# Optimization experiments

Measured on AMD Instinct MI355X. Metric: run time of the kernel, lower is better.

Reference implementation:

```python
import jax, jax.numpy as jnp
import numpy as np

B, S, VD, MD = 32, 2048, 512, 512
AD = max(VD, MD)


def setup_inputs() -> dict:
    key = jax.random.key(0)
    k1, k2, k3, k4, k5, k6 = jax.random.split(key, 6)
    query = jax.random.normal(k1, (B, VD), dtype=jnp.float32)
    keys = jax.random.normal(k2, (B, S, MD), dtype=jnp.float32)
    mask = jax.random.randint(k3, (B, S), 0, 2).astype(jnp.bool_)
    # torch Linear weight layout: [out, in]
    W1 = jax.random.normal(k4, (AD, VD), dtype=jnp.float32) * (1.0 / np.sqrt(VD))
    W2 = jax.random.normal(k5, (AD, MD), dtype=jnp.float32) * (1.0 / np.sqrt(MD))
    v = jax.random.normal(k6, (AD,), dtype=jnp.float32) * (1.0 / np.sqrt(AD))
    return {"query": query, "keys": keys, "mask": mask, "W1": W1, "W2": W2, "v": v}


def reference(query, keys, mask, W1, W2, v):
    # w1_query: [B, 1, AD]; w2_keys: [B, S, AD]
    w1_query = jnp.einsum('bd,ad->ba', query, W1)[:, None, :]
    w2_keys = jnp.einsum('bsd,ad->bsa', keys, W2)
    combined = jnp.tanh(w1_query + w2_keys)            # [B, S, AD]
    scores = jnp.einsum('bsa,a->bs', combined, v)      # [B, S]
    scores = jnp.where(mask, scores, -jnp.inf)
    attn_weights = jax.nn.softmax(scores, axis=-1)
    return attn_weights
```

## Files before the change

### kernel.cpp

```cpp
#include <hip/hip_runtime.h>
#include <math.h>

#define BB 32
#define SS 2048
#define DD 512
#define AD 512

#define BM 128
#define BN 128
#define BK 64

typedef __bf16 bf16;
typedef __attribute__((ext_vector_type(8))) __bf16 bf16x8;
typedef __attribute__((ext_vector_type(4))) __bf16 bf16x4;
typedef __attribute__((ext_vector_type(4))) float floatx4;

__device__ inline void async16(const void* g, void* l) {
    __builtin_amdgcn_global_load_lds(
        (const __attribute__((address_space(1))) unsigned int*)g,
        (__attribute__((address_space(3))) unsigned int*)l, 16, 0, 0);
}

__global__ void mask_probe_kernel(const unsigned char* __restrict__ m8,
                                  int* __restrict__ flag) {
    int t = threadIdx.x + blockIdx.x * 256;
    int any = 0;
    for (int i = t; i < BB * SS; i += gridDim.x * 256) {
        if ((i & 3) && m8[i]) any = 1;
    }
    if (__any(any)) {
        if ((threadIdx.x & 63) == 0) atomicOr(flag, 1);
    }
}

__global__ void convert_kernel(const float* __restrict__ src,
                               bf16* __restrict__ dst, int n8) {
    int i = threadIdx.x + blockIdx.x * 256;
    if (i >= n8) return;
    const float4* s4 = (const float4*)src + (size_t)i * 2;
    float4 x = s4[0], y = s4[1];
    bf16x8 o;
    o[0] = (bf16)x.x; o[1] = (bf16)x.y; o[2] = (bf16)x.z; o[3] = (bf16)x.w;
    o[4] = (bf16)y.x; o[5] = (bf16)y.y; o[6] = (bf16)y.z; o[7] = (bf16)y.w;
    *(bf16x8*)(dst + (size_t)i * 8) = o;
}

__global__ void w1q_kernel(const float* __restrict__ query,
                           const float* __restrict__ W1,
                           float* __restrict__ w1q) {
    int b = blockIdx.y;
    int a = blockIdx.x * 4 + (threadIdx.x >> 6);
    int lane = threadIdx.x & 63;
    const float4* q4 = (const float4*)(query + (size_t)b * DD) + lane * 2;
    const float4* w4 = (const float4*)(W1 + (size_t)a * DD) + lane * 2;
    float4 qa = q4[0], qb = q4[1];
    float4 wa = w4[0], wb = w4[1];
    float acc = qa.x * wa.x + qa.y * wa.y + qa.z * wa.z + qa.w * wa.w
              + qb.x * wb.x + qb.y * wb.y + qb.z * wb.z + qb.w * wb.w;
#pragma unroll
    for (int off = 32; off > 0; off >>= 1) acc += __shfl_down(acc, off);
    if (lane == 0) w1q[(size_t)b * AD + a] = acc;
}

__global__ __launch_bounds__(256, 4)
void gemm_scores_mfma(const bf16* __restrict__ keysb,
                      const bf16* __restrict__ W2b,
                      const float* __restrict__ w1q,
                      const float* __restrict__ v,
                      float* __restrict__ partial, int tiles_y) {
    __shared__ bf16 a_lds[BM * BK];
    __shared__ bf16 b_lds[BN * BK];
    __shared__ float s_red[BM];

    const int t    = threadIdx.x;
    const int lane = t & 63;
    const int w    = t >> 6;
    const int ml   = lane & 15;
    const int kg   = lane >> 4;
    const int b    = blockIdx.z;
    const int s0   = blockIdx.x * BM;
    const int a0   = blockIdx.y * BN;
    const int m_off = (w & 1) * 64;
    const int n_off = (w >> 1) * 64;

    const bf16* Ablk = keysb + ((size_t)b * SS + s0) * DD;
    const bf16* Bblk = W2b + (size_t)a0 * DD;

    if (t < BM) s_red[t] = 0.f;

    floatx4 acc[4][4];
#pragma unroll
    for (int mi = 0; mi < 4; ++mi)
#pragma unroll
        for (int ni = 0; ni < 4; ++ni)
            acc[mi][ni] = (floatx4)(0.f);

    const int rr = lane >> 3;
    const int cc = lane & 7;

    for (int chunk = 0; chunk < DD / BK; ++chunk) {
        const int d0 = chunk * BK;
#pragma unroll
        for (int i = 0; i < 4; ++i) {
            int r  = w * 32 + i * 8 + rr;
            int cs = cc ^ (r & 7);
            const bf16* ga = Ablk + (size_t)r * DD + d0 + cs * 8;
            const bf16* gb = Bblk + (size_t)r * DD + d0 + cs * 8;
            async16(ga, &a_lds[(w * 32 + i * 8) * BK]);
            async16(gb, &b_lds[(w * 32 + i * 8) * BK]);
        }
        __syncthreads();

#pragma unroll
        for (int ks = 0; ks < 2; ++ks) {
            bf16x8 af[4], bfr[4];
#pragma unroll
            for (int mi = 0; mi < 4; ++mi) {
                int R = m_off + mi * 16 + ml;
                int c = (ks * 4 + kg) ^ (R & 7);
                af[mi] = *(const bf16x8*)&a_lds[R * BK + c * 8];
            }
#pragma unroll
            for (int ni = 0; ni < 4; ++ni) {
                int R = n_off + ni * 16 + ml;
                int c = (ks * 4 + kg) ^ (R & 7);
                bfr[ni] = *(const bf16x8*)&b_lds[R * BK + c * 8];
            }
#pragma unroll
            for (int mi = 0; mi < 4; ++mi)
#pragma unroll
                for (int ni = 0; ni < 4; ++ni)
                    acc[mi][ni] = __builtin_amdgcn_mfma_f32_16x16x32_bf16(
                        af[mi], bfr[ni], acc[mi][ni], 0, 0, 0);
        }
        __syncthreads();
    }

    float w1qa[4], va[4];
#pragma unroll
    for (int ni = 0; ni < 4; ++ni) {
        int a = a0 + n_off + ni * 16 + ml;
        w1qa[ni] = w1q[(size_t)b * AD + a];
        va[ni]   = v[a];
    }
#pragma unroll
    for (int mi = 0; mi < 4; ++mi) {
#pragma unroll
        for (int reg = 0; reg < 4; ++reg) {
            float p = 0.f;
#pragma unroll
            for (int ni = 0; ni < 4; ++ni) {
                float x = acc[mi][ni][reg] + w1qa[ni];
                float th = 1.f - 2.f / (1.f + __expf(2.f * x));
                p = fmaf(th, va[ni], p);
            }
            p += __shfl_xor(p, 1);
            p += __shfl_xor(p, 2);
            p += __shfl_xor(p, 4);
            p += __shfl_xor(p, 8);
            if (ml == 0)
                atomicAdd(&s_red[m_off + mi * 16 + kg * 4 + reg], p);
        }
    }
    __syncthreads();
    if (t < BM)
        partial[(((size_t)b * SS) + s0 + t) * (size_t)tiles_y + blockIdx.y] = s_red[t];
}

#define FBK 32
#define FLDK (FBK + 8)
__global__ __launch_bounds__(256, 2)
void gemm_scores_fallback(const float* __restrict__ keys,
                          const float* __restrict__ W2,
                          const float* __restrict__ w1q,
                          const float* __restrict__ v,
                          float* __restrict__ partial) {
    __shared__ bf16 a_lds[BM][FLDK];
    __shared__ bf16 b_lds[BN][FLDK];
    __shared__ float s_red[BM];

    const int t    = threadIdx.x;
    const int lane = t & 63;
    const int w    = t >> 6;
    const int ml   = lane & 15;
    const int kg   = lane >> 4;
    const int b    = blockIdx.z;
    const int s0   = blockIdx.x * BM;
    const int a0   = blockIdx.y * BN;
    const int m_off = (w & 1) * 64;
    const int n_off = (w >> 1) * 64;

    const float* Ablk = keys + ((size_t)b * SS + s0) * DD;
    const float* Bblk = W2 + (size_t)a0 * DD;

    if (t < BM) s_red[t] = 0.f;

    floatx4 acc[4][4];
#pragma unroll
    for (int mi = 0; mi < 4; ++mi)
#pragma unroll
        for (int ni = 0; ni < 4; ++ni)
            acc[mi][ni] = (floatx4)(0.f);

    float4 ga[4], gb[4];
#pragma unroll
    for (int i = 0; i < 4; ++i) {
        int idx = t + 256 * i;
        int r = idx >> 3, c = idx & 7;
        ga[i] = *(const float4*)(Ablk + (size_t)r * DD + c * 4);
        gb[i] = *(const float4*)(Bblk + (size_t)r * DD + c * 4);
    }

    for (int chunk = 0; chunk < DD / FBK; ++chunk) {
        __syncthreads();
#pragma unroll
        for (int i = 0; i < 4; ++i) {
            int idx = t + 256 * i;
            int r = idx >> 3, c = idx & 7;
            bf16x4 pa, pb;
            pa[0] = (bf16)ga[i].x; pa[1] = (bf16)ga[i].y;
            pa[2] = (bf16)ga[i].z; pa[3] = (bf16)ga[i].w;
            pb[0] = (bf16)gb[i].x; pb[1] = (bf16)gb[i].y;
            pb[2] = (bf16)gb[i].z; pb[3] = (bf16)gb[i].w;
            *(bf16x4*)&a_lds[r][c * 4] = pa;
            *(bf16x4*)&b_lds[r][c * 4] = pb;
        }
        __syncthreads();
        if (chunk < DD / FBK - 1) {
            int d0 = (chunk + 1) * FBK;
#pragma unroll
            for (int i = 0; i < 4; ++i) {
                int idx = t + 256 * i;
                int r = idx >> 3, c = idx & 7;
                ga[i] = *(const float4*)(Ablk + (size_t)r * DD + d0 + c * 4);
                gb[i] = *(const float4*)(Bblk + (size_t)r * DD + d0 + c * 4);
            }
        }
        bf16x8 af[4], bfr[4];
#pragma unroll
        for (int mi = 0; mi < 4; ++mi)
            af[mi] = *(const bf16x8*)&a_lds[m_off + mi * 16 + ml][kg * 8];
#pragma unroll
        for (int ni = 0; ni < 4; ++ni)
            bfr[ni] = *(const bf16x8*)&b_lds[n_off + ni * 16 + ml][kg * 8];
#pragma unroll
        for (int mi = 0; mi < 4; ++mi)
#pragma unroll
            for (int ni = 0; ni < 4; ++ni)
                acc[mi][ni] = __builtin_amdgcn_mfma_f32_16x16x32_bf16(
                    af[mi], bfr[ni], acc[mi][ni], 0, 0, 0);
    }

    float w1qa[4], va[4];
#pragma unroll
    for (int ni = 0; ni < 4; ++ni) {
        int a = a0 + n_off + ni * 16 + ml;
        w1qa[ni] = w1q[(size_t)b * AD + a];
        va[ni]   = v[a];
    }
#pragma unroll
    for (int mi = 0; mi < 4; ++mi) {
#pragma unroll
        for (int reg = 0; reg < 4; ++reg) {
            float p = 0.f;
#pragma unroll
            for (int ni = 0; ni < 4; ++ni) {
                float x = acc[mi][ni][reg] + w1qa[ni];
                float th = 1.f - 2.f / (1.f + __expf(2.f * x));
                p = fmaf(th, va[ni], p);
            }
            p += __shfl_xor(p, 1);
            p += __shfl_xor(p, 2);
            p += __shfl_xor(p, 4);
            p += __shfl_xor(p, 8);
            if (ml == 0)
                atomicAdd(&s_red[m_off + mi * 16 + kg * 4 + reg], p);
        }
    }
    __syncthreads();
    if (t < BM)
        partial[(((size_t)b * SS) + s0 + t) * 4 + blockIdx.y] = s_red[t];
}

__global__ void softmax_kernel(const float* __restrict__ partial,
                               const int* __restrict__ mask_i32,
                               const unsigned char* __restrict__ mask_u8,
                               const int* __restrict__ flag,
                               float* __restrict__ out) {
    const int b = blockIdx.x;
    const int t = threadIdx.x;
    __shared__ float rmax[4], rsum[4];
    const int wid = t >> 6, lane = t & 63;

    float sv[8]; int mv[8];
    const int bytes = (*flag != 0);
#pragma unroll
    for (int k = 0; k < 8; ++k) {
        int i = t + 256 * k;
        float4 p4 = *(const float4*)(partial + ((size_t)b * SS + i) * 4);
        sv[k] = (p4.x + p4.y) + (p4.z + p4.w);
        mv[k] = bytes ? (int)mask_u8[(size_t)b * SS + i]
                      : mask_i32[(size_t)b * SS + i];
    }

    float mx = -INFINITY;
#pragma unroll
    for (int k = 0; k < 8; ++k) mx = fmaxf(mx, mv[k] ? sv[k] : -INFINITY);
#pragma unroll
    for (int off = 32; off > 0; off >>= 1) mx = fmaxf(mx, __shfl_xor(mx, off));
    if (lane == 0) rmax[wid] = mx;
    __syncthreads();
    mx = fmaxf(fmaxf(rmax[0], rmax[1]), fmaxf(rmax[2], rmax[3]));

    float ev[8]; float sum = 0.f;
#pragma unroll
    for (int k = 0; k < 8; ++k) {
        ev[k] = mv[k] ? __expf(sv[k] - mx) : 0.f;
        sum += ev[k];
    }
#pragma unroll
    for (int off = 32; off > 0; off >>= 1) sum += __shfl_xor(sum, off);
    if (lane == 0) rsum[wid] = sum;
    __syncthreads();
    sum = (rsum[0] + rsum[1]) + (rsum[2] + rsum[3]);
    float inv = 1.f / sum;
#pragma unroll
    for (int k = 0; k < 8; ++k)
        out[(size_t)b * SS + t + 256 * k] = ev[k] * inv;
}

extern "C" void kernel_launch(void* const* d_in, const int* in_sizes, int n_in,
                              void* d_out, int out_size, void* d_ws, size_t ws_size,
                              hipStream_t stream) {
    const float* query = (const float*)d_in[0];
    const float* keys  = (const float*)d_in[1];
    const void*  mask  = d_in[2];
    const float* W1    = (const float*)d_in[3];
    const float* W2    = (const float*)d_in[4];
    const float* v     = (const float*)d_in[5];
    float* out = (float*)d_out;

    char* wsb = (char*)d_ws;
    int*   flag    = (int*)wsb;
    float* w1q     = (float*)(wsb + 256);
    float* partial = (float*)(wsb + 256 + 65536);
    bf16*  keysb   = (bf16*)(wsb + 256 + 65536 + 1048576);
    bf16*  W2b     = (bf16*)(wsb + 256 + 65536 + 1048576 + (size_t)BB * SS * DD * 2);
    size_t need = 256 + 65536 + 1048576 + (size_t)BB * SS * DD * 2 + (size_t)AD * DD * 2;

    hipMemsetAsync(flag, 0, 4, stream);
    mask_probe_kernel<<<64, 256, 0, stream>>>((const unsigned char*)mask, flag);
    w1q_kernel<<<dim3(AD / 4, BB), 256, 0, stream>>>(query, W1, w1q);

    if (ws_size >= need) {
        int nk8 = BB * SS * DD / 8;
        int nw8 = AD * DD / 8;
        convert_kernel<<<(nk8 + 255) / 256, 256, 0, stream>>>(keys, keysb, nk8);
        convert_kernel<<<(nw8 + 255) / 256, 256, 0, stream>>>(W2, W2b, nw8);
        gemm_scores_mfma<<<dim3(SS / BM, AD / BN, BB), 256, 0, stream>>>(
            keysb, W2b, w1q, v, partial, AD / BN);
    } else {
        gemm_scores_fallback<<<dim3(SS / BM, AD / BN, BB), 256, 0, stream>>>(
            keys, W2, w1q, v, partial);
    }
    softmax_kernel<<<BB, 256, 0, stream>>>(partial, (const int*)mask,
                                           (const unsigned char*)mask, flag, out);
}
```

Baseline: 266.9 us.

## Double-buffer LDS tiles in MFMA GEMM and reorder grid for A-tile reuse

The MFMA scores GEMM now uses two LDS buffers with a K-chunk of 32, issuing async global-to-LDS loads for the next chunk while computing on the current one. This replaces the previous load-sync-compute pattern, which exposed memory latency on every chunk. The grid is also reordered so that the four AD tiles sharing one keys tile are launched next to each other, which should improve L2 reuse of keys. The costs are more chunk iterations, each with its own barrier, and a hardcoded tiles_y of 4. The loop still has a single barrier per chunk, so it relies on the async LDS writes for chunk c+1 having completed when that barrier is reached.

```diff
diff --git a/kernel.cpp b/kernel.cpp
--- a/kernel.cpp
+++ b/kernel.cpp
@@ -8,7 +8,7 @@
 
 #define BM 128
 #define BN 128
-#define BK 64
+#define BK 32
 
 typedef __bf16 bf16;
 typedef __attribute__((ext_vector_type(8))) __bf16 bf16x8;
@@ -67,9 +67,9 @@
                       const bf16* __restrict__ W2b,
                       const float* __restrict__ w1q,
                       const float* __restrict__ v,
-                      float* __restrict__ partial, int tiles_y) {
-    __shared__ bf16 a_lds[BM * BK];
-    __shared__ bf16 b_lds[BN * BK];
+                      float* __restrict__ partial) {
+    __shared__ bf16 a_lds[2][BM * BK];
+    __shared__ bf16 b_lds[2][BN * BK];
     __shared__ float s_red[BM];
 
     const int t    = threadIdx.x;
@@ -78,8 +78,8 @@
     const int ml   = lane & 15;
     const int kg   = lane >> 4;
     const int b    = blockIdx.z;
-    const int s0   = blockIdx.x * BM;
-    const int a0   = blockIdx.y * BN;
+    const int a0   = blockIdx.x * BN;
+    const int s0   = blockIdx.y * BM;
     const int m_off = (w & 1) * 64;
     const int n_off = (w >> 1) * 64;
 
@@ -95,44 +95,51 @@
         for (int ni = 0; ni < 4; ++ni)
             acc[mi][ni] = (floatx4)(0.f);
 
-    const int rr = lane >> 3;
-    const int cc = lane & 7;
-
-    for (int chunk = 0; chunk < DD / BK; ++chunk) {
-        const int d0 = chunk * BK;
-#pragma unroll
-        for (int i = 0; i < 4; ++i) {
-            int r  = w * 32 + i * 8 + rr;
-            int cs = cc ^ (r & 7);
-            const bf16* ga = Ablk + (size_t)r * DD + d0 + cs * 8;
-            const bf16* gb = Bblk + (size_t)r * DD + d0 + cs * 8;
-            async16(ga, &a_lds[(w * 32 + i * 8) * BK]);
-            async16(gb, &b_lds[(w * 32 + i * 8) * BK]);
-        }
-        __syncthreads();
-
-#pragma unroll
-        for (int ks = 0; ks < 2; ++ks) {
-            bf16x8 af[4], bfr[4];
-#pragma unroll
-            for (int mi = 0; mi < 4; ++mi) {
-                int R = m_off + mi * 16 + ml;
-                int c = (ks * 4 + kg) ^ (R & 7);
-                af[mi] = *(const bf16x8*)&a_lds[R * BK + c * 8];
+    const int NCHUNK = DD / BK;
+
+#pragma unroll
+    for (int i = 0; i < 2; ++i) {
+        int lin = w * 128 + i * 64 + lane;
+        int r = lin >> 2, cc = lin & 3, cs = cc ^ (r & 3);
+        async16(Ablk + (size_t)r * DD + cs * 8, &a_lds[0][(w * 128 + i * 64) * 8]);
+        async16(Bblk + (size_t)r * DD + cs * 8, &b_lds[0][(w * 128 + i * 64) * 8]);
+    }
+    __syncthreads();
+
+    for (int c = 0; c < NCHUNK; ++c) {
+        const int cur = c & 1;
+        if (c + 1 < NCHUNK) {
+            const int d0 = (c + 1) * BK;
+            const int nxt = (c + 1) & 1;
+#pragma unroll
+            for (int i = 0; i < 2; ++i) {
+                int lin = w * 128 + i * 64 + lane;
+                int r = lin >> 2, cc = lin & 3, cs = cc ^ (r & 3);
+                async16(Ablk + (size_t)r * DD + d0 + cs * 8,
+                        &a_lds[nxt][(w * 128 + i * 64) * 8]);
+                async16(Bblk + (size_t)r * DD + d0 + cs * 8,
+                        &b_lds[nxt][(w * 128 + i * 64) * 8]);
             }
-#pragma unroll
-            for (int ni = 0; ni < 4; ++ni) {
-                int R = n_off + ni * 16 + ml;
-                int c = (ks * 4 + kg) ^ (R & 7);
-                bfr[ni] = *(const bf16x8*)&b_lds[R * BK + c * 8];
-            }
-#pragma unroll
-            for (int mi = 0; mi < 4; ++mi)
-#pragma unroll
-                for (int ni = 0; ni < 4; ++ni)
-                    acc[mi][ni] = __builtin_amdgcn_mfma_f32_16x16x32_bf16(
-                        af[mi], bfr[ni], acc[mi][ni], 0, 0, 0);
-        }
+        }
+
+        bf16x8 af[4], bfr[4];
+#pragma unroll
+        for (int mi = 0; mi < 4; ++mi) {
+            int R = m_off + mi * 16 + ml;
+            af[mi] = *(const bf16x8*)&a_lds[cur][R * BK + (kg ^ (R & 3)) * 8];
+        }
+#pragma unroll
+        for (int ni = 0; ni < 4; ++ni) {
+            int R = n_off + ni * 16 + ml;
+            bfr[ni] = *(const bf16x8*)&b_lds[cur][R * BK + (kg ^ (R & 3)) * 8];
+        }
+#pragma unroll
+        for (int mi = 0; mi < 4; ++mi)
+#pragma unroll
+            for (int ni = 0; ni < 4; ++ni)
+                acc[mi][ni] = __builtin_amdgcn_mfma_f32_16x16x32_bf16(
+                    af[mi], bfr[ni], acc[mi][ni], 0, 0, 0);
+
         __syncthreads();
     }
 
@@ -164,7 +171,7 @@
     }
     __syncthreads();
     if (t < BM)
-        partial[(((size_t)b * SS) + s0 + t) * (size_t)tiles_y + blockIdx.y] = s_red[t];
+        partial[(((size_t)b * SS) + s0 + t) * 4 + blockIdx.x] = s_red[t];
 }
 
 #define FBK 32
@@ -357,8 +364,8 @@
         int nw8 = AD * DD / 8;
         convert_kernel<<<(nk8 + 255) / 256, 256, 0, stream>>>(keys, keysb, nk8);
         convert_kernel<<<(nw8 + 255) / 256, 256, 0, stream>>>(W2, W2b, nw8);
-        gemm_scores_mfma<<<dim3(SS / BM, AD / BN, BB), 256, 0, stream>>>(
-            keysb, W2b, w1q, v, partial, AD / BN);
+        gemm_scores_mfma<<<dim3(AD / BN, SS / BM, BB), 256, 0, stream>>>(
+            keysb, W2b, w1q, v, partial);
     } else {
         gemm_scores_fallback<<<dim3(SS / BM, AD / BN, BB), 256, 0, stream>>>(
             keys, W2, w1q, v, partial);
```

Result: slower. 276.4 us (+3.6%).

## Fuse prep kernels, swizzle GEMM block order, drop LDS score reduction

Applied to the files above, without the earlier changes.

Merges bf16 conversion, mask probing and query projection into a single prep launch. The GEMM now uses a 1D grid with grouped block ordering so blocks sharing a keys tile run close together, and writes per-wave partial scores into 8 slots instead of reducing through shared-memory atomics. The softmax sums 8 partials. The fallback path launches the fused prep with too few blocks, so it hits only the convert branch and writes into workspace it cannot hold.

```diff
diff --git a/kernel.cpp b/kernel.cpp
--- a/kernel.cpp
+++ b/kernel.cpp
@@ -21,45 +21,55 @@
         (__attribute__((address_space(3))) unsigned int*)l, 16, 0, 0);
 }
 
-__global__ void mask_probe_kernel(const unsigned char* __restrict__ m8,
-                                  int* __restrict__ flag) {
-    int t = threadIdx.x + blockIdx.x * 256;
-    int any = 0;
-    for (int i = t; i < BB * SS; i += gridDim.x * 256) {
-        if ((i & 3) && m8[i]) any = 1;
-    }
-    if (__any(any)) {
-        if ((threadIdx.x & 63) == 0) atomicOr(flag, 1);
-    }
-}
-
-__global__ void convert_kernel(const float* __restrict__ src,
-                               bf16* __restrict__ dst, int n8) {
-    int i = threadIdx.x + blockIdx.x * 256;
-    if (i >= n8) return;
-    const float4* s4 = (const float4*)src + (size_t)i * 2;
-    float4 x = s4[0], y = s4[1];
-    bf16x8 o;
-    o[0] = (bf16)x.x; o[1] = (bf16)x.y; o[2] = (bf16)x.z; o[3] = (bf16)x.w;
-    o[4] = (bf16)y.x; o[5] = (bf16)y.y; o[6] = (bf16)y.z; o[7] = (bf16)y.w;
-    *(bf16x8*)(dst + (size_t)i * 8) = o;
-}
-
-__global__ void w1q_kernel(const float* __restrict__ query,
-                           const float* __restrict__ W1,
-                           float* __restrict__ w1q) {
-    int b = blockIdx.y;
-    int a = blockIdx.x * 4 + (threadIdx.x >> 6);
-    int lane = threadIdx.x & 63;
-    const float4* q4 = (const float4*)(query + (size_t)b * DD) + lane * 2;
-    const float4* w4 = (const float4*)(W1 + (size_t)a * DD) + lane * 2;
-    float4 qa = q4[0], qb = q4[1];
-    float4 wa = w4[0], wb = w4[1];
-    float acc = qa.x * wa.x + qa.y * wa.y + qa.z * wa.z + qa.w * wa.w
-              + qb.x * wb.x + qb.y * wb.y + qb.z * wb.z + qb.w * wb.w;
-#pragma unroll
-    for (int off = 32; off > 0; off >>= 1) acc += __shfl_down(acc, off);
-    if (lane == 0) w1q[(size_t)b * AD + a] = acc;
+#define NK8 (BB * SS * DD / 8)
+#define NW8 (AD * DD / 8)
+#define NCV ((NK8 + NW8) / 256)
+__global__ void prep_kernel(const float* __restrict__ keys,
+                            const float* __restrict__ W2,
+                            bf16* __restrict__ keysb,
+                            bf16* __restrict__ W2b,
+                            const unsigned char* __restrict__ m8,
+                            int* __restrict__ flag,
+                            const float* __restrict__ query,
+                            const float* __restrict__ W1,
+                            float* __restrict__ w1q) {
+    const int bid = blockIdx.x;
+    if (bid < NCV) {
+        int i = threadIdx.x + bid * 256;
+        const float* src;
+        bf16* dst;
+        int j;
+        if (i < NK8) { src = keys; dst = keysb; j = i; }
+        else         { src = W2;   dst = W2b;   j = i - NK8; }
+        const float4* s4 = (const float4*)src + (size_t)j * 2;
+        float4 x = s4[0], y = s4[1];
+        bf16x8 o;
+        o[0] = (bf16)x.x; o[1] = (bf16)x.y; o[2] = (bf16)x.z; o[3] = (bf16)x.w;
+        o[4] = (bf16)y.x; o[5] = (bf16)y.y; o[6] = (bf16)y.z; o[7] = (bf16)y.w;
+        *(bf16x8*)(dst + (size_t)j * 8) = o;
+    } else if (bid < NCV + 64) {
+        int t = threadIdx.x + (bid - NCV) * 256;
+        int any = 0;
+        for (int i = t; i < BB * SS; i += 64 * 256)
+            if ((i & 3) && m8[i]) any = 1;
+        if (__any(any)) {
+            if ((threadIdx.x & 63) == 0) atomicOr(flag, 1);
+        }
+    } else {
+        int id = bid - NCV - 64;
+        int b = id >> 7;
+        int a = (id & 127) * 4 + (threadIdx.x >> 6);
+        int lane = threadIdx.x & 63;
+        const float4* q4 = (const float4*)(query + (size_t)b * DD) + lane * 2;
+        const float4* w4 = (const float4*)(W1 + (size_t)a * DD) + lane * 2;
+        float4 qa = q4[0], qb = q4[1];
+        float4 wa = w4[0], wb = w4[1];
+        float acc = qa.x * wa.x + qa.y * wa.y + qa.z * wa.z + qa.w * wa.w
+                  + qb.x * wb.x + qb.y * wb.y + qb.z * wb.z + qb.w * wb.w;
+#pragma unroll
+        for (int off = 32; off > 0; off >>= 1) acc += __shfl_down(acc, off);
+        if (lane == 0) w1q[(size_t)b * AD + a] = acc;
+    }
 }
 
 __global__ __launch_bounds__(256, 4)
@@ -67,27 +77,31 @@
                       const bf16* __restrict__ W2b,
                       const float* __restrict__ w1q,
                       const float* __restrict__ v,
-                      float* __restrict__ partial, int tiles_y) {
+                      float* __restrict__ partial) {
     __shared__ bf16 a_lds[BM * BK];
     __shared__ bf16 b_lds[BN * BK];
-    __shared__ float s_red[BM];
 
     const int t    = threadIdx.x;
     const int lane = t & 63;
     const int w    = t >> 6;
     const int ml   = lane & 15;
     const int kg   = lane >> 4;
-    const int b    = blockIdx.z;
-    const int s0   = blockIdx.x * BM;
-    const int a0   = blockIdx.y * BN;
+
+    const int lin    = blockIdx.x;
+    const int x8     = lin & 7;
+    const int hi     = lin >> 3;
+    const int a_tile = hi & 3;
+    const int kt     = x8 + ((hi >> 2) << 3);
+    const int b      = kt >> 4;
+    const int s0     = (kt & 15) * BM;
+    const int a0     = a_tile * BN;
+
     const int m_off = (w & 1) * 64;
     const int n_off = (w >> 1) * 64;
 
     const bf16* Ablk = keysb + ((size_t)b * SS + s0) * DD;
     const bf16* Bblk = W2b + (size_t)a0 * DD;
 
-    if (t < BM) s_red[t] = 0.f;
-
     floatx4 acc[4][4];
 #pragma unroll
     for (int mi = 0; mi < 4; ++mi)
@@ -95,19 +109,18 @@
         for (int ni = 0; ni < 4; ++ni)
             acc[mi][ni] = (floatx4)(0.f);
 
-    const int rr = lane >> 3;
-    const int cc = lane & 7;
-
-    for (int chunk = 0; chunk < DD / BK; ++chunk) {
-        const int d0 = chunk * BK;
+    const int NCHUNK = DD / BK;
+    for (int c = 0; c < NCHUNK; ++c) {
+        const int d0 = c * BK;
+        __syncthreads();
 #pragma unroll
         for (int i = 0; i < 4; ++i) {
-            int r  = w * 32 + i * 8 + rr;
-            int cs = cc ^ (r & 7);
-            const bf16* ga = Ablk + (size_t)r * DD + d0 + cs * 8;
-            const bf16* gb = Bblk + (size_t)r * DD + d0 + cs * 8;
-            async16(ga, &a_lds[(w * 32 + i * 8) * BK]);
-            async16(gb, &b_lds[(w * 32 + i * 8) * BK]);
+            int lin2 = t + 256 * i;
+            int r = lin2 >> 3, cc = lin2 & 7, cs = cc ^ (r & 7);
+            async16(Ablk + (size_t)r * DD + d0 + cs * 8,
+                    &a_lds[(256 * i + w * 64) * 8]);
+            async16(Bblk + (size_t)r * DD + d0 + cs * 8,
+                    &b_lds[(256 * i + w * 64) * 8]);
         }
         __syncthreads();
 
@@ -117,14 +130,14 @@
 #pragma unroll
             for (int mi = 0; mi < 4; ++mi) {
                 int R = m_off + mi * 16 + ml;
-                int c = (ks * 4 + kg) ^ (R & 7);
-                af[mi] = *(const bf16x8*)&a_lds[R * BK + c * 8];
+                int pos = (ks * 4 + kg) ^ (R & 7);
+                af[mi] = *(const bf16x8*)&a_lds[R * BK + pos * 8];
             }
 #pragma unroll
             for (int ni = 0; ni < 4; ++ni) {
                 int R = n_off + ni * 16 + ml;
-                int c = (ks * 4 + kg) ^ (R & 7);
-                bfr[ni] = *(const bf16x8*)&b_lds[R * BK + c * 8];
+                int pos = (ks * 4 + kg) ^ (R & 7);
+                bfr[ni] = *(const bf16x8*)&b_lds[R * BK + pos * 8];
             }
 #pragma unroll
             for (int mi = 0; mi < 4; ++mi)
@@ -133,7 +146,6 @@
                     acc[mi][ni] = __builtin_amdgcn_mfma_f32_16x16x32_bf16(
                         af[mi], bfr[ni], acc[mi][ni], 0, 0, 0);
         }
-        __syncthreads();
     }
 
     float w1qa[4], va[4];
@@ -143,6 +155,7 @@
         w1qa[ni] = w1q[(size_t)b * AD + a];
         va[ni]   = v[a];
     }
+    const int slot = a_tile * 2 + (w >> 1);
 #pragma unroll
     for (int mi = 0; mi < 4; ++mi) {
 #pragma unroll
@@ -158,13 +171,12 @@
             p += __shfl_xor(p, 2);
             p += __shfl_xor(p, 4);
             p += __shfl_xor(p, 8);
-            if (ml == 0)
-                atomicAdd(&s_red[m_off + mi * 16 + kg * 4 + reg], p);
-        }
-    }
-    __syncthreads();
-    if (t < BM)
-        partial[(((size_t)b * SS) + s0 + t) * (size_t)tiles_y + blockIdx.y] = s_red[t];
+            if (ml == 0) {
+                int row = m_off + mi * 16 + kg * 4 + reg;
+                partial[((size_t)b * SS + s0 + row) * 8 + slot] = p;
+            }
+        }
+    }
 }
 
 #define FBK 32
@@ -279,7 +291,7 @@
     }
     __syncthreads();
     if (t < BM)
-        partial[(((size_t)b * SS) + s0 + t) * 4 + blockIdx.y] = s_red[t];
+        partial[(((size_t)b * SS) + s0 + t) * 8 + blockIdx.y * 2] = s_red[t];
 }
 
 __global__ void softmax_kernel(const float* __restrict__ partial,
@@ -297,8 +309,9 @@
 #pragma unroll
     for (int k = 0; k < 8; ++k) {
         int i = t + 256 * k;
-        float4 p4 = *(const float4*)(partial + ((size_t)b * SS + i) * 4);
-        sv[k] = (p4.x + p4.y) + (p4.z + p4.w);
+        const float4* p4 = (const float4*)(partial + ((size_t)b * SS + i) * 8);
+        float4 pa = p4[0], pb = p4[1];
+        sv[k] = ((pa.x + pa.y) + (pa.z + pa.w)) + ((pb.x + pb.y) + (pb.z + pb.w));
         mv[k] = bytes ? (int)mask_u8[(size_t)b * SS + i]
                       : mask_i32[(size_t)b * SS + i];
     }
@@ -344,22 +357,20 @@
     int*   flag    = (int*)wsb;
     float* w1q     = (float*)(wsb + 256);
     float* partial = (float*)(wsb + 256 + 65536);
-    bf16*  keysb   = (bf16*)(wsb + 256 + 65536 + 1048576);
-    bf16*  W2b     = (bf16*)(wsb + 256 + 65536 + 1048576 + (size_t)BB * SS * DD * 2);
-    size_t need = 256 + 65536 + 1048576 + (size_t)BB * SS * DD * 2 + (size_t)AD * DD * 2;
+    bf16*  keysb   = (bf16*)(wsb + 256 + 65536 + 2097152);
+    bf16*  W2b     = (bf16*)(wsb + 256 + 65536 + 2097152 + (size_t)BB * SS * DD * 2);
+    size_t need = 256 + 65536 + 2097152 + (size_t)BB * SS * DD * 2 + (size_t)AD * DD * 2;
 
     hipMemsetAsync(flag, 0, 4, stream);
-    mask_probe_kernel<<<64, 256, 0, stream>>>((const unsigned char*)mask, flag);
-    w1q_kernel<<<dim3(AD / 4, BB), 256, 0, stream>>>(query, W1, w1q);
-
     if (ws_size >= need) {
-        int nk8 = BB * SS * DD / 8;
-        int nw8 = AD * DD / 8;
-        convert_kernel<<<(nk8 + 255) / 256, 256, 0, stream>>>(keys, keysb, nk8);
-        convert_kernel<<<(nw8 + 255) / 256, 256, 0, stream>>>(W2, W2b, nw8);
-        gemm_scores_mfma<<<dim3(SS / BM, AD / BN, BB), 256, 0, stream>>>(
-            keysb, W2b, w1q, v, partial, AD / BN);
+        prep_kernel<<<NCV + 64 + 4096, 256, 0, stream>>>(
+            keys, W2, keysb, W2b, (const unsigned char*)mask, flag, query, W1, w1q);
+        gemm_scores_mfma<<<(SS / BM) * (AD / BN) * BB, 256, 0, stream>>>(
+            keysb, W2b, w1q, v, partial);
     } else {
+        hipMemsetAsync(partial, 0, (size_t)BB * SS * 8 * 4, stream);
+        prep_kernel<<<64 + 4096, 256, 0, stream>>>(
+            keys, W2, keysb, W2b, (const unsigned char*)mask, flag, query, W1, w1q);
         gemm_scores_fallback<<<dim3(SS / BM, AD / BN, BB), 256, 0, stream>>>(
             keys, W2, w1q, v, partial);
     }
```

Result: no change. 263.6 us (-1.2%).
